# Kernel tuning notes

Measured on AMD Instinct MI355X. Metric: run time of the kernel, lower is better.

## Reference

```python
import jax, jax.numpy as jnp
import numpy as np


def setup_inputs() -> dict:
    key = jax.random.key(0)
    k_x, k_adj, k_w1, k_b1, k_w2, k_b2 = jax.random.split(key, 6)
    B, S, N, HD = 16, 2048, 64, 32
    x = jax.random.normal(k_x, (B, S, N), dtype=jnp.float32)
    adj = jax.random.uniform(k_adj, (N, N), dtype=jnp.float32)
    # module forces diagonal to 1.0 at init
    adj = adj.at[jnp.arange(N), jnp.arange(N)].set(1.0)
    fc1_w = jax.random.normal(k_w1, (HD, 1), dtype=jnp.float32) * (1.0 / np.sqrt(1.0))
    fc1_b = jax.random.normal(k_b1, (HD,), dtype=jnp.float32) * 0.02
    fc2_w = jax.random.normal(k_w2, (HD, 2 * HD), dtype=jnp.float32) * (1.0 / np.sqrt(2 * HD))
    fc2_b = jax.random.normal(k_b2, (HD,), dtype=jnp.float32) * 0.02
    return {"x": x, "adj": adj, "fc1_w": fc1_w, "fc1_b": fc1_b,
            "fc2_w": fc2_w, "fc2_b": fc2_b}


def reference(x, adj, fc1_w, fc1_b, fc2_w, fc2_b):
    B, S, N = x.shape
    HD = fc1_w.shape[0]
    # row-normalized adjacency
    adj_norm = adj / (adj.sum(axis=1, keepdims=True) + 1e-8)  # [N, N]
    # fc1: Linear(1 -> HD) on x[..., None]; equivalent to outer product + bias
    h = jax.nn.relu(x[..., None] * fc1_w[:, 0] + fc1_b)       # [B, S, N, HD]
    # adjacency-weighted aggregation over variables
    agg = jnp.einsum('ij,bsjf->bsif', adj_norm, h)            # [B, S, N, HD]
    # fc2: Linear(2*HD -> HD) on concat([h, agg])
    h2 = jax.nn.relu(jnp.concatenate([h, agg], axis=-1) @ fc2_w.T + fc2_b)  # [B, S, N, HD]
    # AdaptiveAvgPool1d(1) over seq after permute(0,2,3,1).reshape(B, N*HD, S)
    z = h2.mean(axis=1).reshape(B, N * HD)                    # [B, N*HD]
    return z
```

## Files before the change

kernel.cpp:

```cpp
#include <hip/hip_runtime.h>

#define BN 16
#define SN 2048
#define NV 64
#define HD 32
#define TCH 8
#define SCHUNK 64
#define NSUB (SCHUNK / TCH)
#define CATP 40

typedef short  bf8_t  __attribute__((ext_vector_type(8)));
typedef __bf16 bfv8   __attribute__((ext_vector_type(8)));
typedef __bf16 bfv4   __attribute__((ext_vector_type(4)));
typedef float  f32x16 __attribute__((ext_vector_type(16)));

#define MFMA32(a, b, c) __builtin_amdgcn_mfma_f32_32x32x16_bf16( \
    __builtin_bit_cast(bf8_t, (a)), __builtin_bit_cast(bf8_t, (b)), (c), 0, 0, 0)

__global__ __launch_bounds__(256, 2) void gnn_mfma(
    const float* __restrict__ x,
    const float* __restrict__ adj,
    const float* __restrict__ w1,
    const float* __restrict__ b1,
    const float* __restrict__ w2,
    const float* __restrict__ b2,
    float* __restrict__ out)
{
    __shared__ float  xs[TCH][NV];
    __shared__ __bf16 catg[TCH][NV][CATP];
    __shared__ float  red[NV * HD];
    __shared__ float  rs[NV];

    const int tid  = threadIdx.x;
    const int w    = tid >> 6;
    const int lane = tid & 63;
    const int l31  = lane & 31;
    const int lh   = lane >> 5;
    const int b    = blockIdx.x >> 5;
    const int chk  = blockIdx.x & 31;
    const int sbase = chk * SCHUNK;

    #pragma unroll
    for (int q = 0; q < (NV * HD) / 256; ++q) red[tid + q * 256] = 0.f;

    if (tid < NV) {
        float s = 0.f;
        const float4* r4 = (const float4*)(adj + tid * NV);
        #pragma unroll
        for (int q = 0; q < NV / 4; ++q) { float4 v = r4[q]; s += v.x + v.y + v.z + v.w; }
        rs[tid] = 1.f / (s + 1e-8f);
    }
    __syncthreads();

    bfv8 an[2][4];
    #pragma unroll
    for (int nt = 0; nt < 2; ++nt) {
        const int i = nt * 32 + l31;
        const float rsi = rs[i];
        #pragma unroll
        for (int kk = 0; kk < 4; ++kk) {
            const int j0 = kk * 16 + lh * 8;
            const float4 a0 = *(const float4*)(adj + i * NV + j0);
            const float4 a1 = *(const float4*)(adj + i * NV + j0 + 4);
            bfv8 v;
            v[0] = (__bf16)(a0.x * rsi); v[1] = (__bf16)(a0.y * rsi);
            v[2] = (__bf16)(a0.z * rsi); v[3] = (__bf16)(a0.w * rsi);
            v[4] = (__bf16)(a1.x * rsi); v[5] = (__bf16)(a1.y * rsi);
            v[6] = (__bf16)(a1.z * rsi); v[7] = (__bf16)(a1.w * rsi);
            an[nt][kk] = v;
        }
    }

    bfv8 wf[4];
    #pragma unroll
    for (int kk = 0; kk < 4; ++kk) {
        const int k0 = kk * 16 + lh * 8;
        const float4 a0 = *(const float4*)(w2 + l31 * (2 * HD) + k0);
        const float4 a1 = *(const float4*)(w2 + l31 * (2 * HD) + k0 + 4);
        bfv8 v;
        v[0] = (__bf16)a0.x; v[1] = (__bf16)a0.y; v[2] = (__bf16)a0.z; v[3] = (__bf16)a0.w;
        v[4] = (__bf16)a1.x; v[5] = (__bf16)a1.y; v[6] = (__bf16)a1.z; v[7] = (__bf16)a1.w;
        wf[kk] = v;
    }

    const float w1f = w1[l31];
    const float b1f = b1[l31];
    const float b2f = b2[l31];
    float w1k[2][8], b1k[2][8];
    #pragma unroll
    for (int kk = 0; kk < 2; ++kk) {
        const int k0 = kk * 16 + lh * 8;
        #pragma unroll
        for (int e = 0; e < 8; ++e) { w1k[kk][e] = w1[k0 + e]; b1k[kk][e] = b1[k0 + e]; }
    }

    f32x16 macc0, macc1;
    #pragma unroll
    for (int r = 0; r < 16; ++r) { macc0[r] = 0.f; macc1[r] = 0.f; }

    for (int t = 0; t < NSUB; ++t) {
        __syncthreads();
        if (tid < 128) {
            ((float4*)&xs[0][0])[tid] =
                ((const float4*)(x + ((size_t)b * SN + sbase + t * TCH) * (size_t)NV))[tid];
        }
        __syncthreads();

        #pragma unroll
        for (int sp = 0; sp < 2; ++sp) {
            const int sl = 2 * w + sp;
            bfv8 a1f[4];
            #pragma unroll
            for (int kk = 0; kk < 4; ++kk) {
                const int j0 = kk * 16 + lh * 8;
                const float4 xa = *(const float4*)&xs[sl][j0];
                const float4 xb = *(const float4*)&xs[sl][j0 + 4];
                bfv8 v;
                v[0] = (__bf16)fmaxf(xa.x * w1f + b1f, 0.f);
                v[1] = (__bf16)fmaxf(xa.y * w1f + b1f, 0.f);
                v[2] = (__bf16)fmaxf(xa.z * w1f + b1f, 0.f);
                v[3] = (__bf16)fmaxf(xa.w * w1f + b1f, 0.f);
                v[4] = (__bf16)fmaxf(xb.x * w1f + b1f, 0.f);
                v[5] = (__bf16)fmaxf(xb.y * w1f + b1f, 0.f);
                v[6] = (__bf16)fmaxf(xb.z * w1f + b1f, 0.f);
                v[7] = (__bf16)fmaxf(xb.w * w1f + b1f, 0.f);
                a1f[kk] = v;
            }
            #pragma unroll
            for (int nt = 0; nt < 2; ++nt) {
                f32x16 c;
                #pragma unroll
                for (int r = 0; r < 16; ++r) c[r] = 0.f;
                #pragma unroll
                for (int kk = 0; kk < 4; ++kk) c = MFMA32(a1f[kk], an[nt][kk], c);
                const int i = nt * 32 + l31;
                #pragma unroll
                for (int g = 0; g < 4; ++g) {
                    const int f0 = g * 8 + 4 * lh;
                    bfv4 pv;
                    pv[0] = (__bf16)c[g * 4 + 0]; pv[1] = (__bf16)c[g * 4 + 1];
                    pv[2] = (__bf16)c[g * 4 + 2]; pv[3] = (__bf16)c[g * 4 + 3];
                    *(bfv4*)&catg[sl][i][f0] = pv;
                }
            }
        }

        #pragma unroll
        for (int p = 0; p < 4; ++p) {
            const int mt = 4 * w + p;
            const int sl = mt >> 1;
            const int ih = mt & 1;
            const int i  = ih * 32 + l31;
            const float xv = xs[sl][i];
            f32x16 c;
            #pragma unroll
            for (int r = 0; r < 16; ++r) c[r] = 0.f;
            #pragma unroll
            for (int kk = 0; kk < 2; ++kk) {
                bfv8 v;
                #pragma unroll
                for (int e = 0; e < 8; ++e)
                    v[e] = (__bf16)fmaxf(xv * w1k[kk][e] + b1k[kk][e], 0.f);
                c = MFMA32(v, wf[kk], c);
            }
            #pragma unroll
            for (int kk = 2; kk < 4; ++kk) {
                bfv8 v = *(const bfv8*)&catg[sl][i][(kk - 2) * 16 + lh * 8];
                c = MFMA32(v, wf[kk], c);
            }
            #pragma unroll
            for (int r = 0; r < 16; ++r) {
                const float h2 = fmaxf(c[r] + b2f, 0.f);
                if (ih == 0) macc0[r] += h2; else macc1[r] += h2;
            }
        }
    }

    #pragma unroll
    for (int r = 0; r < 16; ++r) {
        const int row = (r & 3) + 8 * (r >> 2) + 4 * lh;
        atomicAdd(&red[row * HD + l31], macc0[r]);
        atomicAdd(&red[(row + 32) * HD + l31], macc1[r]);
    }
    __syncthreads();
    const float inv = 1.f / (float)SN;
    #pragma unroll
    for (int q = 0; q < (NV * HD) / 256; ++q) {
        const int e = tid + q * 256;
        atomicAdd(out + (size_t)b * (NV * HD) + e, red[e] * inv);
    }
}

extern "C" void kernel_launch(void* const* d_in, const int* in_sizes, int n_in,
                              void* d_out, int out_size, void* d_ws, size_t ws_size,
                              hipStream_t stream) {
    const float* x   = (const float*)d_in[0];
    const float* adj = (const float*)d_in[1];
    const float* w1  = (const float*)d_in[2];
    const float* b1  = (const float*)d_in[3];
    const float* w2  = (const float*)d_in[4];
    const float* b2  = (const float*)d_in[5];
    float* out = (float*)d_out;

    hipMemsetAsync(out, 0, (size_t)out_size * sizeof(float), stream);
    gnn_mfma<<<dim3(BN * 32), dim3(256), 0, stream>>>(x, adj, w1, b1, w2, b2, out);
}
```

Measured before the change: 115.4 us.

## Restructure GNN kernel into per-wave sequence slices with partial-sum reduction

Each wave now owns its own 8-step sequence slice with a private x buffer and concat scratch, which removes the block-wide barriers inside the main loop. The grid grows to 1024 blocks and occupancy is raised to 3 blocks per CU. Normalized adjacency fragments move from registers to LDS to relieve register pressure. The fc2 product is transposed so the bias is folded into the accumulator init. Global atomics are replaced by per-block partial buffers in the workspace plus a separate reduce kernel, falling back to atomics when the workspace is too small; this adds a second launch and extra partial-sum traffic to global memory.

```diff
diff --git a/kernel.cpp b/kernel.cpp
--- a/kernel.cpp
+++ b/kernel.cpp
@@ -4,45 +4,51 @@
 #define SN 2048
 #define NV 64
 #define HD 32
-#define TCH 8
-#define SCHUNK 64
-#define NSUB (SCHUNK / TCH)
-#define CATP 40
-
-typedef short  bf8_t  __attribute__((ext_vector_type(8)));
-typedef __bf16 bfv8   __attribute__((ext_vector_type(8)));
-typedef __bf16 bfv4   __attribute__((ext_vector_type(4)));
+#define SPW 8
+#define SPB (SPW * 4)
+#define NCHUNK (SN / SPB)
+#define CATP 36
+
+typedef short  bf8i  __attribute__((ext_vector_type(8)));
+typedef __bf16 bfv8  __attribute__((ext_vector_type(8)));
+typedef __bf16 bfv4  __attribute__((ext_vector_type(4)));
 typedef float  f32x16 __attribute__((ext_vector_type(16)));
+typedef float  f32x4  __attribute__((ext_vector_type(4)));
 
 #define MFMA32(a, b, c) __builtin_amdgcn_mfma_f32_32x32x16_bf16( \
-    __builtin_bit_cast(bf8_t, (a)), __builtin_bit_cast(bf8_t, (b)), (c), 0, 0, 0)
-
-__global__ __launch_bounds__(256, 2) void gnn_mfma(
+    __builtin_bit_cast(bf8i, (a)), __builtin_bit_cast(bf8i, (b)), (c), 0, 0, 0)
+
+__global__ __launch_bounds__(256, 3) void gnn_main(
     const float* __restrict__ x,
     const float* __restrict__ adj,
     const float* __restrict__ w1,
     const float* __restrict__ b1,
     const float* __restrict__ w2,
     const float* __restrict__ b2,
-    float* __restrict__ out)
+    float* __restrict__ out,
+    float* __restrict__ partial,
+    int use_partial)
 {
-    __shared__ float  xs[TCH][NV];
-    __shared__ __bf16 catg[TCH][NV][CATP];
-    __shared__ float  red[NV * HD];
-    __shared__ float  rs[NV];
+    __shared__ __bf16 anf[8][64][8];
+    __shared__ float  red[HD][NV];
+    __shared__ float  xs[4][4][NV];
+    __shared__ __bf16 catg[4][NV][CATP];
+    __shared__ float  w1s[HD], b1s[HD], b2s[HD], rs[NV];
 
     const int tid  = threadIdx.x;
     const int w    = tid >> 6;
     const int lane = tid & 63;
     const int l31  = lane & 31;
     const int lh   = lane >> 5;
-    const int b    = blockIdx.x >> 5;
-    const int chk  = blockIdx.x & 31;
-    const int sbase = chk * SCHUNK;
-
-    #pragma unroll
-    for (int q = 0; q < (NV * HD) / 256; ++q) red[tid + q * 256] = 0.f;
-
+    const int b    = blockIdx.x >> 6;
+    const int chk  = blockIdx.x & (NCHUNK - 1);
+    const int sbase = chk * SPB + w * SPW;
+
+    {
+        float* rf = &red[0][0];
+        #pragma unroll
+        for (int q = 0; q < (HD * NV) / 256; ++q) rf[tid + q * 256] = 0.f;
+    }
     if (tid < NV) {
         float s = 0.f;
         const float4* r4 = (const float4*)(adj + tid * NV);
@@ -50,25 +56,25 @@
         for (int q = 0; q < NV / 4; ++q) { float4 v = r4[q]; s += v.x + v.y + v.z + v.w; }
         rs[tid] = 1.f / (s + 1e-8f);
     }
+    if (tid < HD) { w1s[tid] = w1[tid]; b1s[tid] = b1[tid]; b2s[tid] = b2[tid]; }
     __syncthreads();
 
-    bfv8 an[2][4];
-    #pragma unroll
-    for (int nt = 0; nt < 2; ++nt) {
-        const int i = nt * 32 + l31;
+    #pragma unroll
+    for (int q = 0; q < 2; ++q) {
+        const int slot = tid + q * 256;
+        const int ntkk = slot >> 6, ln = slot & 63;
+        const int nt = ntkk >> 2, kk = ntkk & 3;
+        const int i  = nt * 32 + (ln & 31);
+        const int j0 = kk * 16 + (ln >> 5) * 8;
         const float rsi = rs[i];
-        #pragma unroll
-        for (int kk = 0; kk < 4; ++kk) {
-            const int j0 = kk * 16 + lh * 8;
-            const float4 a0 = *(const float4*)(adj + i * NV + j0);
-            const float4 a1 = *(const float4*)(adj + i * NV + j0 + 4);
-            bfv8 v;
-            v[0] = (__bf16)(a0.x * rsi); v[1] = (__bf16)(a0.y * rsi);
-            v[2] = (__bf16)(a0.z * rsi); v[3] = (__bf16)(a0.w * rsi);
-            v[4] = (__bf16)(a1.x * rsi); v[5] = (__bf16)(a1.y * rsi);
-            v[6] = (__bf16)(a1.z * rsi); v[7] = (__bf16)(a1.w * rsi);
-            an[nt][kk] = v;
-        }
+        const float4 a0 = *(const float4*)(adj + i * NV + j0);
+        const float4 a1 = *(const float4*)(adj + i * NV + j0 + 4);
+        bfv8 v;
+        v[0] = (__bf16)(a0.x * rsi); v[1] = (__bf16)(a0.y * rsi);
+        v[2] = (__bf16)(a0.z * rsi); v[3] = (__bf16)(a0.w * rsi);
+        v[4] = (__bf16)(a1.x * rsi); v[5] = (__bf16)(a1.y * rsi);
+        v[6] = (__bf16)(a1.z * rsi); v[7] = (__bf16)(a1.w * rsi);
+        *(bfv8*)&anf[ntkk][ln][0] = v;
     }
 
     bfv8 wf[4];
@@ -85,110 +91,147 @@
 
     const float w1f = w1[l31];
     const float b1f = b1[l31];
-    const float b2f = b2[l31];
-    float w1k[2][8], b1k[2][8];
-    #pragma unroll
-    for (int kk = 0; kk < 2; ++kk) {
-        const int k0 = kk * 16 + lh * 8;
-        #pragma unroll
-        for (int e = 0; e < 8; ++e) { w1k[kk][e] = w1[k0 + e]; b1k[kk][e] = b1[k0 + e]; }
-    }
 
     f32x16 macc0, macc1;
     #pragma unroll
     for (int r = 0; r < 16; ++r) { macc0[r] = 0.f; macc1[r] = 0.f; }
 
-    for (int t = 0; t < NSUB; ++t) {
-        __syncthreads();
-        if (tid < 128) {
-            ((float4*)&xs[0][0])[tid] =
-                ((const float4*)(x + ((size_t)b * SN + sbase + t * TCH) * (size_t)NV))[tid];
-        }
-        __syncthreads();
-
-        #pragma unroll
-        for (int sp = 0; sp < 2; ++sp) {
-            const int sl = 2 * w + sp;
-            bfv8 a1f[4];
+    __syncthreads();
+
+    float* xw = &xs[w][0][0];
+
+    for (int g = 0; g < SPW / 4; ++g) {
+        ((float4*)xw)[lane] =
+            ((const float4*)(x + ((size_t)b * SN + sbase + g * 4) * (size_t)NV))[lane];
+
+        #pragma unroll
+        for (int sg = 0; sg < 4; ++sg) {
+            const float* xr = xw + sg * NV;
+
+            bfv8 af[4];
             #pragma unroll
             for (int kk = 0; kk < 4; ++kk) {
                 const int j0 = kk * 16 + lh * 8;
-                const float4 xa = *(const float4*)&xs[sl][j0];
-                const float4 xb = *(const float4*)&xs[sl][j0 + 4];
+                const f32x4 xa = *(const f32x4*)(xr + j0);
+                const f32x4 xb = *(const f32x4*)(xr + j0 + 4);
                 bfv8 v;
-                v[0] = (__bf16)fmaxf(xa.x * w1f + b1f, 0.f);
-                v[1] = (__bf16)fmaxf(xa.y * w1f + b1f, 0.f);
-                v[2] = (__bf16)fmaxf(xa.z * w1f + b1f, 0.f);
-                v[3] = (__bf16)fmaxf(xa.w * w1f + b1f, 0.f);
-                v[4] = (__bf16)fmaxf(xb.x * w1f + b1f, 0.f);
-                v[5] = (__bf16)fmaxf(xb.y * w1f + b1f, 0.f);
-                v[6] = (__bf16)fmaxf(xb.z * w1f + b1f, 0.f);
-                v[7] = (__bf16)fmaxf(xb.w * w1f + b1f, 0.f);
-                a1f[kk] = v;
+                v[0] = (__bf16)fmaxf(xa[0] * w1f + b1f, 0.f);
+                v[1] = (__bf16)fmaxf(xa[1] * w1f + b1f, 0.f);
+                v[2] = (__bf16)fmaxf(xa[2] * w1f + b1f, 0.f);
+                v[3] = (__bf16)fmaxf(xa[3] * w1f + b1f, 0.f);
+                v[4] = (__bf16)fmaxf(xb[0] * w1f + b1f, 0.f);
+                v[5] = (__bf16)fmaxf(xb[1] * w1f + b1f, 0.f);
+                v[6] = (__bf16)fmaxf(xb[2] * w1f + b1f, 0.f);
+                v[7] = (__bf16)fmaxf(xb[3] * w1f + b1f, 0.f);
+                af[kk] = v;
             }
+
             #pragma unroll
             for (int nt = 0; nt < 2; ++nt) {
                 f32x16 c;
                 #pragma unroll
                 for (int r = 0; r < 16; ++r) c[r] = 0.f;
                 #pragma unroll
-                for (int kk = 0; kk < 4; ++kk) c = MFMA32(a1f[kk], an[nt][kk], c);
+                for (int kk = 0; kk < 4; ++kk) {
+                    const bfv8 bn = *(const bfv8*)&anf[nt * 4 + kk][lane][0];
+                    c = MFMA32(af[kk], bn, c);
+                }
                 const int i = nt * 32 + l31;
                 #pragma unroll
-                for (int g = 0; g < 4; ++g) {
-                    const int f0 = g * 8 + 4 * lh;
+                for (int gq = 0; gq < 4; ++gq) {
+                    const int f0 = gq * 8 + 4 * lh;
                     bfv4 pv;
-                    pv[0] = (__bf16)c[g * 4 + 0]; pv[1] = (__bf16)c[g * 4 + 1];
-                    pv[2] = (__bf16)c[g * 4 + 2]; pv[3] = (__bf16)c[g * 4 + 3];
-                    *(bfv4*)&catg[sl][i][f0] = pv;
+                    pv[0] = (__bf16)c[4 * gq + 0]; pv[1] = (__bf16)c[4 * gq + 1];
+                    pv[2] = (__bf16)c[4 * gq + 2]; pv[3] = (__bf16)c[4 * gq + 3];
+                    *(bfv4*)&catg[w][i][f0] = pv;
+                }
+            }
+
+            #pragma unroll
+            for (int ih = 0; ih < 2; ++ih) {
+                const int i2 = ih * 32 + l31;
+                const float xi = xr[i2];
+                f32x16 c;
+                #pragma unroll
+                for (int gq = 0; gq < 4; ++gq) {
+                    const f32x4 bv = *(const f32x4*)&b2s[gq * 8 + 4 * lh];
+                    c[4 * gq + 0] = bv[0]; c[4 * gq + 1] = bv[1];
+                    c[4 * gq + 2] = bv[2]; c[4 * gq + 3] = bv[3];
+                }
+                #pragma unroll
+                for (int kk = 0; kk < 2; ++kk) {
+                    const int f0 = kk * 16 + lh * 8;
+                    const f32x4 wa = *(const f32x4*)&w1s[f0];
+                    const f32x4 wb = *(const f32x4*)&w1s[f0 + 4];
+                    const f32x4 ba = *(const f32x4*)&b1s[f0];
+                    const f32x4 bb = *(const f32x4*)&b1s[f0 + 4];
+                    bfv8 hv;
+                    hv[0] = (__bf16)fmaxf(xi * wa[0] + ba[0], 0.f);
+                    hv[1] = (__bf16)fmaxf(xi * wa[1] + ba[1], 0.f);
+                    hv[2] = (__bf16)fmaxf(xi * wa[2] + ba[2], 0.f);
+                    hv[3] = (__bf16)fmaxf(xi * wa[3] + ba[3], 0.f);
+                    hv[4] = (__bf16)fmaxf(xi * wb[0] + bb[0], 0.f);
+                    hv[5] = (__bf16)fmaxf(xi * wb[1] + bb[1], 0.f);
+                    hv[6] = (__bf16)fmaxf(xi * wb[2] + bb[2], 0.f);
+                    hv[7] = (__bf16)fmaxf(xi * wb[3] + bb[3], 0.f);
+                    c = MFMA32(wf[kk], hv, c);
+                }
+                #pragma unroll
+                for (int kk = 2; kk < 4; ++kk) {
+                    const int fa0 = (kk - 2) * 16 + lh * 8;
+                    const bfv4 lo = *(const bfv4*)&catg[w][i2][fa0];
+                    const bfv4 hi = *(const bfv4*)&catg[w][i2][fa0 + 4];
+                    bfv8 bv;
+                    bv[0] = lo[0]; bv[1] = lo[1]; bv[2] = lo[2]; bv[3] = lo[3];
+                    bv[4] = hi[0]; bv[5] = hi[1]; bv[6] = hi[2]; bv[7] = hi[3];
+                    c = MFMA32(wf[kk], bv, c);
+                }
+                if (ih == 0) {
+                    #pragma unroll
+                    for (int r = 0; r < 16; ++r) macc0[r] += fmaxf(c[r], 0.f);
+                } else {
+                    #pragma unroll
+                    for (int r = 0; r < 16; ++r) macc1[r] += fmaxf(c[r], 0.f);
                 }
             }
         }
-
-        #pragma unroll
-        for (int p = 0; p < 4; ++p) {
-            const int mt = 4 * w + p;
-            const int sl = mt >> 1;
-            const int ih = mt & 1;
-            const int i  = ih * 32 + l31;
-            const float xv = xs[sl][i];
-            f32x16 c;
-            #pragma unroll
-            for (int r = 0; r < 16; ++r) c[r] = 0.f;
-            #pragma unroll
-            for (int kk = 0; kk < 2; ++kk) {
-                bfv8 v;
-                #pragma unroll
-                for (int e = 0; e < 8; ++e)
-                    v[e] = (__bf16)fmaxf(xv * w1k[kk][e] + b1k[kk][e], 0.f);
-                c = MFMA32(v, wf[kk], c);
-            }
-            #pragma unroll
-            for (int kk = 2; kk < 4; ++kk) {
-                bfv8 v = *(const bfv8*)&catg[sl][i][(kk - 2) * 16 + lh * 8];
-                c = MFMA32(v, wf[kk], c);
-            }
-            #pragma unroll
-            for (int r = 0; r < 16; ++r) {
-                const float h2 = fmaxf(c[r] + b2f, 0.f);
-                if (ih == 0) macc0[r] += h2; else macc1[r] += h2;
-            }
-        }
     }
 
     #pragma unroll
     for (int r = 0; r < 16; ++r) {
         const int row = (r & 3) + 8 * (r >> 2) + 4 * lh;
-        atomicAdd(&red[row * HD + l31], macc0[r]);
-        atomicAdd(&red[(row + 32) * HD + l31], macc1[r]);
+        atomicAdd(&red[row][l31], macc0[r]);
+        atomicAdd(&red[row][l31 + 32], macc1[r]);
     }
     __syncthreads();
-    const float inv = 1.f / (float)SN;
-    #pragma unroll
-    for (int q = 0; q < (NV * HD) / 256; ++q) {
-        const int e = tid + q * 256;
-        atomicAdd(out + (size_t)b * (NV * HD) + e, red[e] * inv);
-    }
+    const float* rf = &red[0][0];
+    if (use_partial) {
+        float* dst = partial + (size_t)blockIdx.x * (NV * HD);
+        #pragma unroll
+        for (int q = 0; q < (HD * NV) / 256; ++q) dst[tid + q * 256] = rf[tid + q * 256];
+    } else {
+        const float inv = 1.f / (float)SN;
+        #pragma unroll
+        for (int q = 0; q < (HD * NV) / 256; ++q) {
+            const int e = tid + q * 256;
+            const int f = e >> 6, i = e & 63;
+            atomicAdd(out + (size_t)b * (NV * HD) + i * HD + f, rf[e] * inv);
+        }
+    }
+}
+
+__global__ __launch_bounds__(256) void gnn_reduce(
+    const float* __restrict__ partial, float* __restrict__ out)
+{
+    const int t = blockIdx.x * 256 + threadIdx.x;
+    const int b = t >> 11;
+    const int e = t & 2047;
+    const float* p = partial + (size_t)b * NCHUNK * 2048 + e;
+    float s = 0.f;
+    #pragma unroll 8
+    for (int c = 0; c < NCHUNK; ++c) s += p[(size_t)c * 2048];
+    const int f = e >> 6, i = e & 63;
+    out[(size_t)b * 2048 + i * HD + f] = s * (1.f / (float)SN);
 }
 
 extern "C" void kernel_launch(void* const* d_in, const int* in_sizes, int n_in,
@@ -202,6 +245,11 @@
     const float* b2  = (const float*)d_in[5];
     float* out = (float*)d_out;
 
-    hipMemsetAsync(out, 0, (size_t)out_size * sizeof(float), stream);
-    gnn_mfma<<<dim3(BN * 32), dim3(256), 0, stream>>>(x, adj, w1, b1, w2, b2, out);
+    const size_t need = (size_t)(BN * NCHUNK) * (NV * HD) * sizeof(float);
+    const int useP = (d_ws != nullptr && ws_size >= need) ? 1 : 0;
+
+    if (!useP) hipMemsetAsync(out, 0, (size_t)out_size * sizeof(float), stream);
+    gnn_main<<<dim3(BN * NCHUNK), dim3(256), 0, stream>>>(
+        x, adj, w1, b1, w2, b2, out, (float*)d_ws, useP);
+    if (useP) gnn_reduce<<<dim3(BN * SN / 256), dim3(256), 0, stream>>>((float*)d_ws, out);
 }
```

Measured after the change: 249.5 us. 2.16x slower.
